# Kernel tuning notes

Hardware: AMD Instinct MI355X
Metric: run time of the kernel (lower is better)

Reference implementation:

```python
import jax, jax.numpy as jnp
import numpy as np

NUM_EXPERTS = 64
TOP_K = 2
AUX_COEF = 0.01
Z_COEF = 0.001
INIT_STD = 0.02


def setup_inputs() -> dict:
    key = jax.random.key(0)
    k1, k2 = jax.random.split(key)
    B, S, D = 4, 4096, 2048
    x = jax.random.normal(k1, (B, S, D), dtype=jnp.float32)
    gate_w = jax.random.normal(k2, (NUM_EXPERTS, D), dtype=jnp.float32) * INIT_STD
    return {"x": x, "gate_w": gate_w}


def reference(x, gate_w):
    B, S, D = x.shape
    E, K = NUM_EXPERTS, TOP_K
    # gate linear: (B,S,D) @ (D,E) -> (B,S,E), cast to fp32 like .float()
    logits = jnp.einsum('bsd,ed->bse', x, gate_w).astype(jnp.float32)
    weights = jax.nn.softmax(logits, axis=-1)
    top_weights, top_indices = jax.lax.top_k(weights, K)
    top_weights = top_weights / jnp.sum(top_weights, axis=-1, keepdims=True)
    # load-balance aux loss (training branch)
    flat_idx = top_indices.reshape(-1)
    tokens_per_expert = jax.ops.segment_sum(
        jnp.ones_like(flat_idx, dtype=jnp.float32), flat_idx, num_segments=E)
    f = tokens_per_expert / (B * S * K)
    P = jnp.mean(weights, axis=(0, 1))
    balance_loss = E * jnp.sum(f * P)
    z_loss = jnp.mean(jnp.square(jax.nn.logsumexp(logits, axis=-1)))
    aux_loss = AUX_COEF * balance_loss + Z_COEF * z_loss
    return top_indices, top_weights, aux_loss
```

## Files before the change

### kernel.cpp

```cpp
#include <hip/hip_runtime.h>
#include <math.h>

#define NTOK 16384
#define DDIM 2048
#define NEXP 64
#define NKQ 8
#define KSLICE 256
#define TPB 128

typedef __attribute__((ext_vector_type(8))) short bf16x8;
typedef __attribute__((ext_vector_type(4))) float f32x4;


__device__ __forceinline__ void split3pk(float a, float b,
                                         unsigned &H, unsigned &M, unsigned &L) {
    asm("v_cvt_pk_bf16_f32 %0, %1, %2" : "=v"(H) : "v"(a), "v"(b));
    float ra = a - __builtin_bit_cast(float, H << 16);
    float rb = b - __builtin_bit_cast(float, H & 0xffff0000u);
    asm("v_cvt_pk_bf16_f32 %0, %1, %2" : "=v"(M) : "v"(ra), "v"(rb));
    float sa = ra - __builtin_bit_cast(float, M << 16);
    float sb = rb - __builtin_bit_cast(float, M & 0xffff0000u);
    asm("v_cvt_pk_bf16_f32 %0, %1, %2" : "=v"(L) : "v"(sa), "v"(sb));
}

__global__ void k_wpack(const float* __restrict__ gw, unsigned short* __restrict__ wp) {
    int idx = blockIdx.x * 256 + threadIdx.x;
    int lane = idx & 63;
    int ks   = (idx >> 6) & 63;
    int eg   = idx >> 12;
    int e  = eg * 16 + (lane & 15);
    int k0 = ks * 32 + (lane >> 4) * 8;
    const float* src = gw + (size_t)e * DDIM + k0;
    uint4 H, M, L;
    split3pk(src[0], src[1], H.x, M.x, L.x);
    split3pk(src[2], src[3], H.y, M.y, L.y);
    split3pk(src[4], src[5], H.z, M.z, L.z);
    split3pk(src[6], src[7], H.w, M.w, L.w);
    size_t fb = ((size_t)ks * 12 + eg * 3) * 512 + lane * 8;
    *(uint4*)(wp + fb)        = H;
    *(uint4*)(wp + fb + 512)  = M;
    *(uint4*)(wp + fb + 1024) = L;
}

__global__ __launch_bounds__(512, 2)
void k_gemm(const float* __restrict__ x, const unsigned short* __restrict__ wp,
            float* __restrict__ part) {
    __shared__ __align__(16) char Ws[49152];

    const int tid  = threadIdx.x;
    const int kq   = blockIdx.x & 7;
    const int tok0 = (blockIdx.x >> 3) * TPB;
    const int lane = tid & 63;
    const int wv   = tid >> 6;
    const int tau  = lane & 15;
    const int kap  = lane >> 4;

    const float* xb = x + (size_t)(tok0 + wv * 16 + tau) * DDIM
                        + kq * KSLICE + kap * 8;
    float4 xf[4][2];
    #pragma unroll
    for (int i = 0; i < 4; ++i) {
        xf[i][0] = *(const float4*)(xb + i * 32);
        xf[i][1] = *(const float4*)(xb + i * 32 + 4);
    }

    const char* wsrc = (const char*)wp + (size_t)(kq * 8) * 12288;
    uint4 wreg[6];
    #pragma unroll
    for (int r = 0; r < 6; ++r)
        wreg[r] = *(const uint4*)(wsrc + (r * 512 + tid) * 16);

    f32x4 acc[4];
    #pragma unroll
    for (int eg = 0; eg < 4; ++eg) acc[eg] = (f32x4){0.f, 0.f, 0.f, 0.f};

    for (int h = 0; h < 2; ++h) {
        if (h) __syncthreads();
        #pragma unroll
        for (int r = 0; r < 6; ++r)
            *(uint4*)(Ws + (r * 512 + tid) * 16) = wreg[r];
        if (h == 0) {
            #pragma unroll
            for (int r = 0; r < 6; ++r)
                wreg[r] = *(const uint4*)(wsrc + 49152 + (r * 512 + tid) * 16);
        }
        __syncthreads();

        #pragma unroll
        for (int ks = 0; ks < 4; ++ks) {
            float4 a = xf[ks][0], b = xf[ks][1];
            uint4 Ah, Am, Al;
            split3pk(a.x, a.y, Ah.x, Am.x, Al.x);
            split3pk(a.z, a.w, Ah.y, Am.y, Al.y);
            split3pk(b.x, b.y, Ah.z, Am.z, Al.z);
            split3pk(b.z, b.w, Ah.w, Am.w, Al.w);
            bf16x8 Ahv = __builtin_bit_cast(bf16x8, Ah);
            bf16x8 Amv = __builtin_bit_cast(bf16x8, Am);
            bf16x8 Alv = __builtin_bit_cast(bf16x8, Al);

            if (h == 0) {
                xf[ks][0] = *(const float4*)(xb + 128 + ks * 32);
                xf[ks][1] = *(const float4*)(xb + 128 + ks * 32 + 4);
            }

            #pragma unroll
            for (int eg = 0; eg < 4; ++eg) {
                const char* wb = Ws + ks * 12288 + eg * 3072 + lane * 16;
                bf16x8 Bh = *(const bf16x8*)(wb);
                bf16x8 Bm = *(const bf16x8*)(wb + 1024);
                bf16x8 Bl = *(const bf16x8*)(wb + 2048);
                acc[eg] = __builtin_amdgcn_mfma_f32_16x16x32_bf16(Ahv, Bh, acc[eg], 0, 0, 0);
                acc[eg] = __builtin_amdgcn_mfma_f32_16x16x32_bf16(Ahv, Bm, acc[eg], 0, 0, 0);
                acc[eg] = __builtin_amdgcn_mfma_f32_16x16x32_bf16(Amv, Bh, acc[eg], 0, 0, 0);
                acc[eg] = __builtin_amdgcn_mfma_f32_16x16x32_bf16(Ahv, Bl, acc[eg], 0, 0, 0);
                acc[eg] = __builtin_amdgcn_mfma_f32_16x16x32_bf16(Alv, Bh, acc[eg], 0, 0, 0);
                acc[eg] = __builtin_amdgcn_mfma_f32_16x16x32_bf16(Amv, Bm, acc[eg], 0, 0, 0);
            }
        }
    }

    float* pb = part + ((size_t)kq * NTOK + tok0 + wv * 16) * 64;
    #pragma unroll
    for (int eg = 0; eg < 4; ++eg)
        #pragma unroll
        for (int j = 0; j < 4; ++j)
            pb[(kap * 4 + j) * 64 + eg * 16 + tau] = acc[eg][j];
}

__global__ __launch_bounds__(256)
void k_reduce(const float* __restrict__ part, float* __restrict__ out,
              float* __restrict__ gcnt, float* __restrict__ gP,
              float* __restrict__ gz) {
    __shared__ float Ps[NEXP], Cnt[NEXP], Zs;
    const int tid = threadIdx.x;
    if (tid < NEXP) { Ps[tid] = 0.f; Cnt[tid] = 0.f; }
    if (tid == 0) Zs = 0.f;
    __syncthreads();

    const int lane = tid & 63;
    const int wv   = tid >> 6;
    const int t0   = blockIdx.x * 16 + wv * 4;

    float v[4][8];
    #pragma unroll
    for (int i = 0; i < 4; ++i)
        #pragma unroll
        for (int q = 0; q < 8; ++q)
            v[i][q] = part[((size_t)q * NTOK + t0 + i) * 64 + lane];

    float Pacc = 0.f, zacc = 0.f;
    #pragma unroll
    for (int i = 0; i < 4; ++i) {
        float l = ((v[i][0] + v[i][1]) + (v[i][2] + v[i][3]))
                + ((v[i][4] + v[i][5]) + (v[i][6] + v[i][7]));
        float mx = l;
        #pragma unroll
        for (int off = 32; off > 0; off >>= 1) mx = fmaxf(mx, __shfl_xor(mx, off));
        float s = expf(l - mx);
        float sum = s;
        #pragma unroll
        for (int off = 32; off > 0; off >>= 1) sum += __shfl_xor(sum, off);
        Pacc += s / sum;

        unsigned long long b1 = __ballot(l == mx);
        int i1 = __ffsll(b1) - 1;
        float l2 = (lane == i1) ? -INFINITY : l;
        float m2 = l2;
        #pragma unroll
        for (int off = 32; off > 0; off >>= 1) m2 = fmaxf(m2, __shfl_xor(m2, off));
        unsigned long long b2 = __ballot(l2 == m2);
        int i2 = __ffsll(b2) - 1;

        if (lane == 0) {
            float s2  = expf(m2 - mx);
            float inv = 1.f / (1.f + s2);
            int gt = t0 + i;
            ((float2*)out)[gt]              = make_float2((float)i1, (float)i2);
            ((float2*)(out + 2 * NTOK))[gt] = make_float2(inv, s2 * inv);
            atomicAdd(&Cnt[i1], 1.f);
            atomicAdd(&Cnt[i2], 1.f);
            float lse = mx + logf(sum);
            zacc += lse * lse;
        }
    }
    atomicAdd(&Ps[lane], Pacc);
    if (lane == 0) atomicAdd(&Zs, zacc);
    __syncthreads();

    if (tid < NEXP) {
        atomicAdd(&gcnt[tid], Cnt[tid]);
        atomicAdd(&gP[tid],   Ps[tid]);
    }
    if (tid == 0) atomicAdd(gz, Zs);
}

__global__ void k_final(const float* __restrict__ ws, float* __restrict__ out) {
    int lane = threadIdx.x;
    float v = ws[lane] * ws[64 + lane];
    #pragma unroll
    for (int off = 32; off > 0; off >>= 1) v += __shfl_xor(v, off);
    if (lane == 0) {
        float bal = 64.f * v / (32768.f * 16384.f);
        float z   = ws[128] / 16384.f;
        out[4 * NTOK] = 0.01f * bal + 0.001f * z;
    }
}

extern "C" void kernel_launch(void* const* d_in, const int* in_sizes, int n_in,
                              void* d_out, int out_size, void* d_ws, size_t ws_size,
                              hipStream_t stream) {
    const float* x  = (const float*)d_in[0];
    const float* gw = (const float*)d_in[1];
    float* out = (float*)d_out;
    float* wsf = (float*)d_ws;
    unsigned short* wp = (unsigned short*)((char*)d_ws + 1024);
    float* part = (float*)((char*)d_ws + (1 << 20));

    hipMemsetAsync(d_ws, 0, 516, stream);
    k_wpack<<<64, 256, 0, stream>>>(gw, wp);
    k_gemm<<<NKQ * (NTOK / TPB), 512, 0, stream>>>(x, wp, part);
    k_reduce<<<NTOK / 16, 256, 0, stream>>>(part, out, wsf, wsf + 64, wsf + 128);
    k_final<<<1, 64, 0, stream>>>(wsf, out);
}
```

Before: 95.14 us.

## Split GEMM K into 16 slices with direct global-to-LDS weight loads

Halves the K slice and token tile per block, giving 16 K-quarters and 64-token, 256-thread blocks with a single LDS stage. The weight tile now goes straight into LDS via global_load_lds instead of being staged through registers, and the two-phase software pipeline is removed. The reduce kernel sums 16 partials instead of 8, so partial-sum traffic doubles in exchange for more parallelism and less register pressure. Summation order changes slightly.

```diff
diff --git a/kernel.cpp b/kernel.cpp
--- a/kernel.cpp
+++ b/kernel.cpp
@@ -4,9 +4,9 @@
 #define NTOK 16384
 #define DDIM 2048
 #define NEXP 64
-#define NKQ 8
-#define KSLICE 256
-#define TPB 128
+#define NKQ 16
+#define KSLICE 128
+#define TPB 64
 
 typedef __attribute__((ext_vector_type(8))) short bf16x8;
 typedef __attribute__((ext_vector_type(4))) float f32x4;
@@ -21,6 +21,10 @@
     float sa = ra - __builtin_bit_cast(float, M << 16);
     float sb = rb - __builtin_bit_cast(float, M & 0xffff0000u);
     asm("v_cvt_pk_bf16_f32 %0, %1, %2" : "=v"(L) : "v"(sa), "v"(sb));
+}
+
+__device__ __forceinline__ void keepf(float4 &v) {
+    asm volatile("" : "+v"(v.x), "+v"(v.y), "+v"(v.z), "+v"(v.w));
 }
 
 __global__ void k_wpack(const float* __restrict__ gw, unsigned short* __restrict__ wp) {
@@ -42,84 +46,79 @@
     *(uint4*)(wp + fb + 1024) = L;
 }
 
-__global__ __launch_bounds__(512, 2)
+__global__ __launch_bounds__(256, 2)
 void k_gemm(const float* __restrict__ x, const unsigned short* __restrict__ wp,
             float* __restrict__ part) {
     __shared__ __align__(16) char Ws[49152];
 
     const int tid  = threadIdx.x;
-    const int kq   = blockIdx.x & 7;
-    const int tok0 = (blockIdx.x >> 3) * TPB;
+    const int kq   = blockIdx.x & 15;
+    const int tok0 = (blockIdx.x >> 4) * TPB;
     const int lane = tid & 63;
-    const int wv   = tid >> 6;
+    const int wvu  = __builtin_amdgcn_readfirstlane(tid >> 6);
     const int tau  = lane & 15;
     const int kap  = lane >> 4;
 
-    const float* xb = x + (size_t)(tok0 + wv * 16 + tau) * DDIM
+    {
+        const char* wsrc = (const char*)wp + (size_t)kq * 49152;
+        #pragma unroll
+        for (int r = 0; r < 12; ++r) {
+            const char* g = wsrc + (size_t)(r * 256 + tid) * 16;
+            char* l = Ws + (size_t)(r * 256 + wvu * 64) * 16;
+            __builtin_amdgcn_global_load_lds(
+                (const __attribute__((address_space(1))) void*)g,
+                (__attribute__((address_space(3))) void*)l, 16, 0, 0);
+        }
+    }
+
+    const float* xb = x + (size_t)(tok0 + wvu * 16 + tau) * DDIM
                         + kq * KSLICE + kap * 8;
-    float4 xf[4][2];
-    #pragma unroll
-    for (int i = 0; i < 4; ++i) {
-        xf[i][0] = *(const float4*)(xb + i * 32);
-        xf[i][1] = *(const float4*)(xb + i * 32 + 4);
-    }
-
-    const char* wsrc = (const char*)wp + (size_t)(kq * 8) * 12288;
-    uint4 wreg[6];
-    #pragma unroll
-    for (int r = 0; r < 6; ++r)
-        wreg[r] = *(const uint4*)(wsrc + (r * 512 + tid) * 16);
+    float4 x0a = *(const float4*)(xb);
+    float4 x0b = *(const float4*)(xb + 4);
+    float4 x1a = *(const float4*)(xb + 32);
+    float4 x1b = *(const float4*)(xb + 36);
+    float4 x2a = *(const float4*)(xb + 64);
+    float4 x2b = *(const float4*)(xb + 68);
+    float4 x3a = *(const float4*)(xb + 96);
+    float4 x3b = *(const float4*)(xb + 100);
+    keepf(x0a); keepf(x0b); keepf(x1a); keepf(x1b);
+    keepf(x2a); keepf(x2b); keepf(x3a); keepf(x3b);
+
+    __syncthreads();
 
     f32x4 acc[4];
     #pragma unroll
     for (int eg = 0; eg < 4; ++eg) acc[eg] = (f32x4){0.f, 0.f, 0.f, 0.f};
 
-    for (int h = 0; h < 2; ++h) {
-        if (h) __syncthreads();
-        #pragma unroll
-        for (int r = 0; r < 6; ++r)
-            *(uint4*)(Ws + (r * 512 + tid) * 16) = wreg[r];
-        if (h == 0) {
-            #pragma unroll
-            for (int r = 0; r < 6; ++r)
-                wreg[r] = *(const uint4*)(wsrc + 49152 + (r * 512 + tid) * 16);
+    #pragma unroll
+    for (int ks = 0; ks < 4; ++ks) {
+        float4 a = (ks == 0) ? x0a : (ks == 1) ? x1a : (ks == 2) ? x2a : x3a;
+        float4 b = (ks == 0) ? x0b : (ks == 1) ? x1b : (ks == 2) ? x2b : x3b;
+        uint4 Ah, Am, Al;
+        split3pk(a.x, a.y, Ah.x, Am.x, Al.x);
+        split3pk(a.z, a.w, Ah.y, Am.y, Al.y);
+        split3pk(b.x, b.y, Ah.z, Am.z, Al.z);
+        split3pk(b.z, b.w, Ah.w, Am.w, Al.w);
+        bf16x8 Ahv = __builtin_bit_cast(bf16x8, Ah);
+        bf16x8 Amv = __builtin_bit_cast(bf16x8, Am);
+        bf16x8 Alv = __builtin_bit_cast(bf16x8, Al);
+
+        #pragma unroll
+        for (int eg = 0; eg < 4; ++eg) {
+            const char* wb = Ws + ks * 12288 + eg * 3072 + lane * 16;
+            bf16x8 Bh = *(const bf16x8*)(wb);
+            bf16x8 Bm = *(const bf16x8*)(wb + 1024);
+            bf16x8 Bl = *(const bf16x8*)(wb + 2048);
+            acc[eg] = __builtin_amdgcn_mfma_f32_16x16x32_bf16(Ahv, Bh, acc[eg], 0, 0, 0);
+            acc[eg] = __builtin_amdgcn_mfma_f32_16x16x32_bf16(Ahv, Bm, acc[eg], 0, 0, 0);
+            acc[eg] = __builtin_amdgcn_mfma_f32_16x16x32_bf16(Amv, Bh, acc[eg], 0, 0, 0);
+            acc[eg] = __builtin_amdgcn_mfma_f32_16x16x32_bf16(Ahv, Bl, acc[eg], 0, 0, 0);
+            acc[eg] = __builtin_amdgcn_mfma_f32_16x16x32_bf16(Alv, Bh, acc[eg], 0, 0, 0);
+            acc[eg] = __builtin_amdgcn_mfma_f32_16x16x32_bf16(Amv, Bm, acc[eg], 0, 0, 0);
         }
-        __syncthreads();
-
-        #pragma unroll
-        for (int ks = 0; ks < 4; ++ks) {
-            float4 a = xf[ks][0], b = xf[ks][1];
-            uint4 Ah, Am, Al;
-            split3pk(a.x, a.y, Ah.x, Am.x, Al.x);
-            split3pk(a.z, a.w, Ah.y, Am.y, Al.y);
-            split3pk(b.x, b.y, Ah.z, Am.z, Al.z);
-            split3pk(b.z, b.w, Ah.w, Am.w, Al.w);
-            bf16x8 Ahv = __builtin_bit_cast(bf16x8, Ah);
-            bf16x8 Amv = __builtin_bit_cast(bf16x8, Am);
-            bf16x8 Alv = __builtin_bit_cast(bf16x8, Al);
-
-            if (h == 0) {
-                xf[ks][0] = *(const float4*)(xb + 128 + ks * 32);
-                xf[ks][1] = *(const float4*)(xb + 128 + ks * 32 + 4);
-            }
-
-            #pragma unroll
-            for (int eg = 0; eg < 4; ++eg) {
-                const char* wb = Ws + ks * 12288 + eg * 3072 + lane * 16;
-                bf16x8 Bh = *(const bf16x8*)(wb);
-                bf16x8 Bm = *(const bf16x8*)(wb + 1024);
-                bf16x8 Bl = *(const bf16x8*)(wb + 2048);
-                acc[eg] = __builtin_amdgcn_mfma_f32_16x16x32_bf16(Ahv, Bh, acc[eg], 0, 0, 0);
-                acc[eg] = __builtin_amdgcn_mfma_f32_16x16x32_bf16(Ahv, Bm, acc[eg], 0, 0, 0);
-                acc[eg] = __builtin_amdgcn_mfma_f32_16x16x32_bf16(Amv, Bh, acc[eg], 0, 0, 0);
-                acc[eg] = __builtin_amdgcn_mfma_f32_16x16x32_bf16(Ahv, Bl, acc[eg], 0, 0, 0);
-                acc[eg] = __builtin_amdgcn_mfma_f32_16x16x32_bf16(Alv, Bh, acc[eg], 0, 0, 0);
-                acc[eg] = __builtin_amdgcn_mfma_f32_16x16x32_bf16(Amv, Bm, acc[eg], 0, 0, 0);
-            }
-        }
-    }
-
-    float* pb = part + ((size_t)kq * NTOK + tok0 + wv * 16) * 64;
+    }
+
+    float* pb = part + ((size_t)kq * NTOK + tok0 + wvu * 16) * 64;
     #pragma unroll
     for (int eg = 0; eg < 4; ++eg)
         #pragma unroll
@@ -127,7 +126,7 @@
             pb[(kap * 4 + j) * 64 + eg * 16 + tau] = acc[eg][j];
 }
 
-__global__ __launch_bounds__(256)
+__global__ __launch_bounds__(256, 2)
 void k_reduce(const float* __restrict__ part, float* __restrict__ out,
               float* __restrict__ gcnt, float* __restrict__ gP,
               float* __restrict__ gz) {
@@ -141,18 +140,17 @@
     const int wv   = tid >> 6;
     const int t0   = blockIdx.x * 16 + wv * 4;
 
-    float v[4][8];
-    #pragma unroll
-    for (int i = 0; i < 4; ++i)
-        #pragma unroll
-        for (int q = 0; q < 8; ++q)
-            v[i][q] = part[((size_t)q * NTOK + t0 + i) * 64 + lane];
+    float l4[4] = {0.f, 0.f, 0.f, 0.f};
+    #pragma unroll
+    for (int q = 0; q < NKQ; ++q)
+        #pragma unroll
+        for (int i = 0; i < 4; ++i)
+            l4[i] += part[((size_t)q * NTOK + t0 + i) * 64 + lane];
 
     float Pacc = 0.f, zacc = 0.f;
     #pragma unroll
     for (int i = 0; i < 4; ++i) {
-        float l = ((v[i][0] + v[i][1]) + (v[i][2] + v[i][3]))
-                + ((v[i][4] + v[i][5]) + (v[i][6] + v[i][7]));
+        float l = l4[i];
         float mx = l;
         #pragma unroll
         for (int off = 32; off > 0; off >>= 1) mx = fmaxf(mx, __shfl_xor(mx, off));
@@ -218,7 +216,7 @@
 
     hipMemsetAsync(d_ws, 0, 516, stream);
     k_wpack<<<64, 256, 0, stream>>>(gw, wp);
-    k_gemm<<<NKQ * (NTOK / TPB), 512, 0, stream>>>(x, wp, part);
+    k_gemm<<<NKQ * (NTOK / TPB), 256, 0, stream>>>(x, wp, part);
     k_reduce<<<NTOK / 16, 256, 0, stream>>>(part, out, wsf, wsf + 64, wsf + 128);
     k_final<<<1, 64, 0, stream>>>(wsf, out);
 }
```

Measured after the change: 83.63 us. -12.1%, faster.
